# Kernel optimization log

Measured on AMD Instinct MI355X. Metric: run time of the kernel, lower is better.

The kernel has to match this reference:

```python
import jax, jax.numpy as jnp
import numpy as np

L, T, DIN, DOUT = 64, 8192, 128, 128

def setup_inputs() -> dict:
    key = jax.random.key(0)
    k1, k2, k3 = jax.random.split(key, 3)
    x = jax.random.normal(k1, (L, T, DIN), dtype=jnp.float32)
    w = jax.random.normal(k2, (L, DIN, DOUT), dtype=jnp.float32)
    b = jax.random.normal(k3, (L, 1, DOUT), dtype=jnp.float32)
    return {"x": x, "w": w, "b": b}

def reference(x, w, b):
    # grouped GEMM: per-layer matmul x[l] @ w[l], fused bias add
    out = jnp.einsum('lti,lio->lto', x, w) + b  # [L, T, DOUT]
    return out
```

## Files before the change

kernel.cpp:

```cpp
#include <hip/hip_runtime.h>
#include <hip/hip_bf16.h>

#define L_N 64
#define T_N 8192
#define K_N 128
#define N_N 128
#define BM  128

typedef __attribute__((ext_vector_type(8))) short short8;
typedef __attribute__((ext_vector_type(4))) float f32x4;

__device__ __forceinline__ unsigned short f2bf(float f) {
    union { float f; unsigned u; } c; c.f = f;
    return (unsigned short)((c.u + 0x7fffu + ((c.u >> 16) & 1u)) >> 16);
}

__global__ __launch_bounds__(256) void wfrag_kernel(const float* __restrict__ w,
                                                    unsigned short* __restrict__ wf) {
    __shared__ float lds[K_N * 129];
    const int l = blockIdx.x;
    const float* wl = w + (size_t)l * (K_N * N_N);
    const int tid = threadIdx.x;
    #pragma unroll
    for (int i = 0; i < 16; ++i) {
        int f = i * 256 + tid;
        float4 v = ((const float4*)wl)[f];
        int k = f >> 5, n = (f & 31) * 4;
        lds[k * 129 + n + 0] = v.x;
        lds[k * 129 + n + 1] = v.y;
        lds[k * 129 + n + 2] = v.z;
        lds[k * 129 + n + 3] = v.w;
    }
    __syncthreads();
    unsigned short* o = wf + (size_t)l * (N_N * K_N);
    #pragma unroll
    for (int c = 0; c < 16; ++c) {
        int chunk = c * 256 + tid;
        int j0   = (chunk & 1) * 4;
        int lane = (chunk >> 1) & 63;
        int kk   = (chunk >> 7) & 3;
        int ni   = chunk >> 9;
        int n  = ni * 16 + (lane & 15);
        int kb = kk * 32 + (lane >> 4) * 8 + j0;
        ushort4 ov;
        ov.x = f2bf(lds[(kb + 0) * 129 + n]);
        ov.y = f2bf(lds[(kb + 1) * 129 + n]);
        ov.z = f2bf(lds[(kb + 2) * 129 + n]);
        ov.w = f2bf(lds[(kb + 3) * 129 + n]);
        ((ushort4*)o)[chunk] = ov;
    }
}

__global__ __launch_bounds__(512, 4) void gl_kernel(const float* __restrict__ x,
                                                    const unsigned short* __restrict__ wf,
                                                    const float* __restrict__ bias,
                                                    float* __restrict__ out) {
    __shared__ __align__(16) char smem[65536];
    unsigned short* xs  = (unsigned short*)smem;
    unsigned short* wsh = (unsigned short*)(smem + 32768);

    const int tid  = threadIdx.x;
    const int lane = tid & 63;
    const int wid  = tid >> 6;
    const int lr   = lane & 15;
    const int lg   = lane >> 4;

    const int bid  = blockIdx.x;
    const int l    = bid >> 6;
    const int tile = bid & 63;
    const float* xg = x + ((size_t)l * T_N + tile * BM) * K_N;
    const unsigned short* wl = wf + (size_t)l * (N_N * K_N);

    #pragma unroll
    for (int i = 0; i < 8; ++i) {
        int f = i * 512 + tid;
        const float4 v = ((const float4*)xg)[f];
        int row = f >> 5;
        int kc  = (f & 31) * 4;
        union { unsigned short s[4]; unsigned long long u; } p;
        p.s[0] = f2bf(v.x); p.s[1] = f2bf(v.y); p.s[2] = f2bf(v.z); p.s[3] = f2bf(v.w);
        int us = (row * K_N + kc) ^ ((row & 7) << 3);
        *(unsigned long long*)&xs[us] = p.u;
    }
    #pragma unroll
    for (int i = 0; i < 4; ++i) {
        int c = i * 512 + tid;
        ((short8*)wsh)[c] = ((const short8*)wl)[c];
    }
    __syncthreads();

    f32x4 acc[8];
    #pragma unroll
    for (int ni = 0; ni < 8; ++ni)
        acc[ni] = (f32x4){0.f, 0.f, 0.f, 0.f};

    const int tbase = wid * 16;
    #pragma unroll
    for (int kk = 0; kk < 4; ++kk) {
        const int row = tbase + lr;
        const short8 xb = *(const short8*)&xs[(row * K_N + kk * 32 + lg * 8) ^ ((row & 7) << 3)];
        short8 wv[8];
        #pragma unroll
        for (int ni = 0; ni < 8; ++ni)
            wv[ni] = ((const short8*)wsh)[(ni * 4 + kk) * 64 + lane];
        #pragma unroll
        for (int ni = 0; ni < 8; ++ni)
            acc[ni] = __builtin_amdgcn_mfma_f32_16x16x32_bf16(wv[ni], xb, acc[ni], 0, 0, 0);
    }

    const float* bl = bias + l * N_N;
    __syncthreads();
    float4* osm = (float4*)smem;
    #pragma unroll
    for (int ni = 0; ni < 8; ++ni) {
        const float4 bv = *(const float4*)(bl + ni * 16 + lg * 4);
        float4 r;
        r.x = acc[ni][0] + bv.x;
        r.y = acc[ni][1] + bv.y;
        r.z = acc[ni][2] + bv.z;
        r.w = acc[ni][3] + bv.w;
        const int row = tbase + lr;
        const int cf4 = ni * 4 + lg;
        osm[row * 32 + (cf4 ^ (row & 7))] = r;
    }
    __syncthreads();
    float4* og = (float4*)(out + ((size_t)l * T_N + tile * BM) * N_N);
    #pragma unroll
    for (int i = 0; i < 8; ++i) {
        int fi = i * 512 + tid;
        int row = fi >> 5, cf4 = fi & 31;
        og[fi] = osm[row * 32 + (cf4 ^ (row & 7))];
    }
}

extern "C" void kernel_launch(void* const* d_in, const int* in_sizes, int n_in,
                              void* d_out, int out_size, void* d_ws, size_t ws_size,
                              hipStream_t stream) {
    const float* x = (const float*)d_in[0];
    const float* w = (const float*)d_in[1];
    const float* b = (const float*)d_in[2];
    float* out = (float*)d_out;
    unsigned short* wf = (unsigned short*)d_ws;

    wfrag_kernel<<<L_N, 256, 0, stream>>>(w, wf);
    gl_kernel<<<L_N * (T_N / BM), 512, 0, stream>>>(x, wf, b, out);
}
```

Baseline: 110.1 us.

## Process multiple row tiles per block with register prefetch of next X tile

Each block now loops over eight consecutive 128-row tiles of one layer. The weight fragments are loaded into LDS once per block, and the next X tile is prefetched into registers while the current tile's MFMAs run. Output is staged per wave in that wave's own slice of LDS and written back in two halves, which removes the block-wide barrier before the store. The intent is to cut redundant weight loads and hide global latency. The trade-off is an eight-fold smaller grid, which lowers occupancy and load balance on a kernel that is already close to bandwidth-bound.

```diff
diff --git a/kernel.cpp b/kernel.cpp
--- a/kernel.cpp
+++ b/kernel.cpp
@@ -6,6 +6,7 @@
 #define K_N 128
 #define N_N 128
 #define BM  128
+#define NT  8
 
 typedef __attribute__((ext_vector_type(8))) short short8;
 typedef __attribute__((ext_vector_type(4))) float f32x4;
@@ -65,71 +66,85 @@
     const int lr   = lane & 15;
     const int lg   = lane >> 4;
 
-    const int bid  = blockIdx.x;
-    const int l    = bid >> 6;
-    const int tile = bid & 63;
-    const float* xg = x + ((size_t)l * T_N + tile * BM) * K_N;
+    const int bid = blockIdx.x;
+    const int l   = bid >> 3;
+    const int sub = bid & 7;
+
     const unsigned short* wl = wf + (size_t)l * (N_N * K_N);
-
-    #pragma unroll
-    for (int i = 0; i < 8; ++i) {
-        int f = i * 512 + tid;
-        const float4 v = ((const float4*)xg)[f];
-        int row = f >> 5;
-        int kc  = (f & 31) * 4;
-        union { unsigned short s[4]; unsigned long long u; } p;
-        p.s[0] = f2bf(v.x); p.s[1] = f2bf(v.y); p.s[2] = f2bf(v.z); p.s[3] = f2bf(v.w);
-        int us = (row * K_N + kc) ^ ((row & 7) << 3);
-        *(unsigned long long*)&xs[us] = p.u;
-    }
     #pragma unroll
     for (int i = 0; i < 4; ++i) {
         int c = i * 512 + tid;
         ((short8*)wsh)[c] = ((const short8*)wl)[c];
     }
-    __syncthreads();
 
-    f32x4 acc[8];
+    const float* bl  = bias + l * N_N;
+    const float* xg0 = x + ((size_t)l * T_N + (size_t)sub * (NT * BM)) * K_N;
+
+    float4 pf[8];
     #pragma unroll
-    for (int ni = 0; ni < 8; ++ni)
-        acc[ni] = (f32x4){0.f, 0.f, 0.f, 0.f};
+    for (int j = 0; j < 8; ++j)
+        pf[j] = ((const float4*)xg0)[j * 512 + tid];
 
-    const int tbase = wid * 16;
-    #pragma unroll
-    for (int kk = 0; kk < 4; ++kk) {
-        const int row = tbase + lr;
-        const short8 xb = *(const short8*)&xs[(row * K_N + kk * 32 + lg * 8) ^ ((row & 7) << 3)];
-        short8 wv[8];
+    for (int it = 0; it < NT; ++it) {
+        __syncthreads();
+        #pragma unroll
+        for (int j = 0; j < 8; ++j) {
+            int f = j * 512 + tid;
+            int row = f >> 5;
+            int kc  = (f & 31) * 4;
+            union { unsigned short s[4]; unsigned long long u; } p;
+            p.s[0] = f2bf(pf[j].x); p.s[1] = f2bf(pf[j].y);
+            p.s[2] = f2bf(pf[j].z); p.s[3] = f2bf(pf[j].w);
+            int us = (row * K_N + kc) ^ ((row & 7) << 3);
+            *(unsigned long long*)&xs[us] = p.u;
+        }
+        __syncthreads();
+
+        if (it + 1 < NT) {
+            const float4* nx = (const float4*)(xg0 + (size_t)(it + 1) * BM * K_N);
+            #pragma unroll
+            for (int j = 0; j < 8; ++j)
+                pf[j] = nx[j * 512 + tid];
+        }
+
+        f32x4 acc[8];
         #pragma unroll
         for (int ni = 0; ni < 8; ++ni)
-            wv[ni] = ((const short8*)wsh)[(ni * 4 + kk) * 64 + lane];
+            acc[ni] = (f32x4){0.f, 0.f, 0.f, 0.f};
+        const int row = wid * 16 + lr;
         #pragma unroll
-        for (int ni = 0; ni < 8; ++ni)
-            acc[ni] = __builtin_amdgcn_mfma_f32_16x16x32_bf16(wv[ni], xb, acc[ni], 0, 0, 0);
-    }
+        for (int kk = 0; kk < 4; ++kk) {
+            const short8 xb = *(const short8*)&xs[(row * K_N + kk * 32 + lg * 8) ^ ((row & 7) << 3)];
+            #pragma unroll
+            for (int ni = 0; ni < 8; ++ni) {
+                const short8 wv = ((const short8*)wsh)[(ni * 4 + kk) * 64 + lane];
+                acc[ni] = __builtin_amdgcn_mfma_f32_16x16x32_bf16(wv, xb, acc[ni], 0, 0, 0);
+            }
+        }
 
-    const float* bl = bias + l * N_N;
-    __syncthreads();
-    float4* osm = (float4*)smem;
-    #pragma unroll
-    for (int ni = 0; ni < 8; ++ni) {
-        const float4 bv = *(const float4*)(bl + ni * 16 + lg * 4);
-        float4 r;
-        r.x = acc[ni][0] + bv.x;
-        r.y = acc[ni][1] + bv.y;
-        r.z = acc[ni][2] + bv.z;
-        r.w = acc[ni][3] + bv.w;
-        const int row = tbase + lr;
-        const int cf4 = ni * 4 + lg;
-        osm[row * 32 + (cf4 ^ (row & 7))] = r;
-    }
-    __syncthreads();
-    float4* og = (float4*)(out + ((size_t)l * T_N + tile * BM) * N_N);
-    #pragma unroll
-    for (int i = 0; i < 8; ++i) {
-        int fi = i * 512 + tid;
-        int row = fi >> 5, cf4 = fi & 31;
-        og[fi] = osm[row * 32 + (cf4 ^ (row & 7))];
+        float4* osm = ((float4*)smem) + wid * 256;
+        float4* og4 = (float4*)(out + ((size_t)l * T_N + (size_t)(sub * NT + it) * BM) * N_N);
+        #pragma unroll
+        for (int h = 0; h < 2; ++h) {
+            #pragma unroll
+            for (int q = 0; q < 4; ++q) {
+                const int ni = h * 4 + q;
+                const float4 bv = *(const float4*)(bl + ni * 16 + lg * 4);
+                float4 r;
+                r.x = acc[ni][0] + bv.x;
+                r.y = acc[ni][1] + bv.y;
+                r.z = acc[ni][2] + bv.z;
+                r.w = acc[ni][3] + bv.w;
+                osm[lr * 16 + ((q * 4 + lg) ^ lr)] = r;
+            }
+            #pragma unroll
+            for (int q2 = 0; q2 < 4; ++q2) {
+                const int fi = q2 * 64 + lane;
+                const int rr = fi >> 4, cc = fi & 15;
+                const float4 v = osm[rr * 16 + (cc ^ rr)];
+                og4[(size_t)(wid * 16 + rr) * 32 + h * 16 + cc] = v;
+            }
+        }
     }
 }
 
@@ -143,5 +158,5 @@
     unsigned short* wf = (unsigned short*)d_ws;
 
     wfrag_kernel<<<L_N, 256, 0, stream>>>(w, wf);
-    gl_kernel<<<L_N * (T_N / BM), 512, 0, stream>>>(x, wf, b, out);
+    gl_kernel<<<L_N * (T_N / BM) / NT, 512, 0, stream>>>(x, wf, b, out);
 }
```

After: 116.2 us. +5.6%, slower.

## Halve row tile, split N across wave pairs, per-wave output staging

Applied to the files above, without the earlier changes.

Row tile drops from 128 to 64, which doubles the grid and shrinks shared memory from 64KB to 48KB. Launch bounds now target 6 blocks per CU. Each pair of waves shares 16 rows and each wave computes half of the 128 output columns, so a wave holds fewer accumulators. The epilogue stages output in a private per-wave shared-memory region and drops the final block-wide barrier, while the weight tile is still reloaded for every block, now twice as often.

```diff
diff --git a/kernel.cpp b/kernel.cpp
--- a/kernel.cpp
+++ b/kernel.cpp
@@ -5,7 +5,7 @@
 #define T_N 8192
 #define K_N 128
 #define N_N 128
-#define BM  128
+#define BM  64
 
 typedef __attribute__((ext_vector_type(8))) short short8;
 typedef __attribute__((ext_vector_type(4))) float f32x4;
@@ -51,28 +51,30 @@
     }
 }
 
-__global__ __launch_bounds__(512, 4) void gl_kernel(const float* __restrict__ x,
+__global__ __launch_bounds__(512, 6) void gl_kernel(const float* __restrict__ x,
                                                     const unsigned short* __restrict__ wf,
                                                     const float* __restrict__ bias,
                                                     float* __restrict__ out) {
-    __shared__ __align__(16) char smem[65536];
+    __shared__ __align__(16) char smem[49152];
     unsigned short* xs  = (unsigned short*)smem;
-    unsigned short* wsh = (unsigned short*)(smem + 32768);
+    unsigned short* wsh = (unsigned short*)(smem + 16384);
 
     const int tid  = threadIdx.x;
     const int lane = tid & 63;
     const int wid  = tid >> 6;
     const int lr   = lane & 15;
     const int lg   = lane >> 4;
+    const int ws   = wid >> 1;
+    const int ch   = wid & 1;
 
     const int bid  = blockIdx.x;
-    const int l    = bid >> 6;
-    const int tile = bid & 63;
-    const float* xg = x + ((size_t)l * T_N + tile * BM) * K_N;
+    const int l    = bid >> 7;
+    const int tile = bid & 127;
+    const float* xg = x + ((size_t)l * T_N + (size_t)tile * BM) * K_N;
     const unsigned short* wl = wf + (size_t)l * (N_N * K_N);
 
     #pragma unroll
-    for (int i = 0; i < 8; ++i) {
+    for (int i = 0; i < 4; ++i) {
         int f = i * 512 + tid;
         const float4 v = ((const float4*)xg)[f];
         int row = f >> 5;
@@ -89,47 +91,43 @@
     }
     __syncthreads();
 
-    f32x4 acc[8];
+    f32x4 acc[4];
     #pragma unroll
-    for (int ni = 0; ni < 8; ++ni)
-        acc[ni] = (f32x4){0.f, 0.f, 0.f, 0.f};
-
-    const int tbase = wid * 16;
+    for (int q = 0; q < 4; ++q)
+        acc[q] = (f32x4){0.f, 0.f, 0.f, 0.f};
+    const int row = ws * 16 + lr;
     #pragma unroll
     for (int kk = 0; kk < 4; ++kk) {
-        const int row = tbase + lr;
         const short8 xb = *(const short8*)&xs[(row * K_N + kk * 32 + lg * 8) ^ ((row & 7) << 3)];
-        short8 wv[8];
         #pragma unroll
-        for (int ni = 0; ni < 8; ++ni)
-            wv[ni] = ((const short8*)wsh)[(ni * 4 + kk) * 64 + lane];
-        #pragma unroll
-        for (int ni = 0; ni < 8; ++ni)
-            acc[ni] = __builtin_amdgcn_mfma_f32_16x16x32_bf16(wv[ni], xb, acc[ni], 0, 0, 0);
+        for (int q = 0; q < 4; ++q) {
+            const int ni = ch * 4 + q;
+            const short8 wv = ((const short8*)wsh)[(ni * 4 + kk) * 64 + lane];
+            acc[q] = __builtin_amdgcn_mfma_f32_16x16x32_bf16(wv, xb, acc[q], 0, 0, 0);
+        }
     }
+    __syncthreads();
 
     const float* bl = bias + l * N_N;
-    __syncthreads();
-    float4* osm = (float4*)smem;
+    float4* osm = (float4*)(smem + wid * 4096);
     #pragma unroll
-    for (int ni = 0; ni < 8; ++ni) {
+    for (int q = 0; q < 4; ++q) {
+        const int ni = ch * 4 + q;
         const float4 bv = *(const float4*)(bl + ni * 16 + lg * 4);
         float4 r;
-        r.x = acc[ni][0] + bv.x;
-        r.y = acc[ni][1] + bv.y;
-        r.z = acc[ni][2] + bv.z;
-        r.w = acc[ni][3] + bv.w;
-        const int row = tbase + lr;
-        const int cf4 = ni * 4 + lg;
-        osm[row * 32 + (cf4 ^ (row & 7))] = r;
+        r.x = acc[q][0] + bv.x;
+        r.y = acc[q][1] + bv.y;
+        r.z = acc[q][2] + bv.z;
+        r.w = acc[q][3] + bv.w;
+        osm[lr * 16 + ((q * 4 + lg) ^ lr)] = r;
     }
-    __syncthreads();
-    float4* og = (float4*)(out + ((size_t)l * T_N + tile * BM) * N_N);
+    float4* og4 = (float4*)(out + ((size_t)l * T_N + (size_t)tile * BM + ws * 16) * N_N);
     #pragma unroll
-    for (int i = 0; i < 8; ++i) {
-        int fi = i * 512 + tid;
-        int row = fi >> 5, cf4 = fi & 31;
-        og[fi] = osm[row * 32 + (cf4 ^ (row & 7))];
+    for (int q2 = 0; q2 < 4; ++q2) {
+        const int fi = q2 * 64 + lane;
+        const int rr = fi >> 4, cc = fi & 15;
+        const float4 v = osm[rr * 16 + (cc ^ rr)];
+        og4[(size_t)rr * 32 + ch * 16 + cc] = v;
     }
 }
 
```

Result: faster. 105.8 us (-3.9%).
